# Performance work log

Measured on AMD Instinct MI355X. Metric: run time of the kernel, lower is better.

## Reference

```python
import jax, jax.numpy as jnp
import numpy as np

N = 100000      # nodes
E = 1_600_000   # edges (avg degree 16)
IN = 128
HID = 128
OUT = 64
C = 7           # num classes == K clusters
BETA = 1.0
NEG_SLOPE = 0.2


def setup_inputs() -> dict:
    key = jax.random.key(0)
    ks = jax.random.split(key, 12)
    x = jax.random.normal(ks[0], (N, IN), jnp.float32)
    edge_index = jax.random.randint(ks[1], (2, E), 0, N, dtype=jnp.int32)
    y = jax.random.randint(ks[2], (N,), 0, C, dtype=jnp.int32)
    C_b_prime = jax.random.normal(ks[3], (C, IN), jnp.float32)
    Q = jax.random.uniform(ks[4], (C, C), jnp.float32, 0.1, 1.0)  # positive, log-safe
    s1 = 1.0 / np.sqrt(IN)
    s2 = 1.0 / np.sqrt(HID)
    W1 = jax.random.uniform(ks[5], (IN, HID), jnp.float32, -s1, s1)
    a_src1 = jax.random.uniform(ks[6], (HID,), jnp.float32, -s2, s2)
    a_dst1 = jax.random.uniform(ks[7], (HID,), jnp.float32, -s2, s2)
    b1 = jnp.zeros((HID,), jnp.float32)
    W2 = jax.random.uniform(ks[8], (HID, OUT), jnp.float32, -s2, s2)
    b2 = jnp.zeros((OUT,), jnp.float32)
    return dict(x=x, edge_index=edge_index, y=y, C_b_prime=C_b_prime, Q=Q,
                W1=W1, a_src1=a_src1, a_dst1=a_dst1, b1=b1, W2=W2, b2=b2)


def _segment_softmax(logits, seg, num):
    m = jax.ops.segment_max(logits, seg, num_segments=num)
    e = jnp.exp(logits - m[seg])
    s = jax.ops.segment_sum(e, seg, num_segments=num)
    return e / (s[seg] + 1e-16)


def _clust_score(feat, cent, beta=BETA):
    # get_clust_score_pytorch: softmax-normalized exp(-beta * ||f - c_k||)
    d = jnp.linalg.norm(feat[:, None, :] - cent[None, :, :], axis=2)  # [N,K]
    sc = jnp.exp(-beta * d) + 1e-10
    return sc / sc.sum(1, keepdims=True)


def _gat_layer1(x, W, a_src, a_dst, b, src, dst):
    h = x @ W                                                   # F_0: [N,HID]
    logits = jax.nn.leaky_relu(h[src] @ a_src + h[dst] @ a_dst, NEG_SLOPE)  # [E]
    alpha = _segment_softmax(logits, dst, N)                    # B_0: [E]
    out = jax.ops.segment_sum(alpha[:, None] * h[src], dst, num_segments=N) + b  # Z_0
    return out, alpha, h


def reference(x, edge_index, y, C_b_prime, Q, W1, a_src1, a_dst1, b1, W2, b2):
    src, dst = edge_index[0], edge_index[1]

    # conv1 (GAT, heads=1) with return_attention_weights
    Z0, B0, F0 = _gat_layer1(x, W1, a_src1, a_dst1, b1, src, dst)
    x1 = jax.nn.elu(Z0)  # dropout p=0.5 in eval mode -> identity

    # ---- get_grad_IB_B_large ----
    y1h = jax.nn.one_hot(y, C, dtype=x.dtype)
    # run_kmeans(Z, y, C) replaced by detached class-mean centroids
    cnt = jax.ops.segment_sum(jnp.ones((N,), x.dtype), y, num_segments=C)
    C_a = jax.lax.stop_gradient(
        jax.ops.segment_sum(Z0, y, num_segments=C) / (cnt[:, None] + 1e-12))
    phi_Z = jax.lax.stop_gradient(_clust_score(Z0, C_a))      # [N,C], detached
    phi_X = _clust_score(x, C_b_prime)                        # [N,C]
    S = jnp.log(phi_X).sum(1)                                 # sum_b log phi_X_b
    diff_b = phi_Z * S[:, None] - y1h @ jnp.log(Q)            # [N,C]
    # U = d phi_Z / d Z (softmax-of-neg-distance Jacobian)
    dZ = Z0[:, None, :] - C_a[None, :, :]                     # [N,C,HID]
    dist = jnp.linalg.norm(dZ, axis=2, keepdims=True) + 1e-12
    g = -BETA * dZ / dist
    U = phi_Z[..., None] * (g - jnp.sum(phi_Z[..., None] * g, axis=1, keepdims=True))
    v = jnp.einsum('nkd,nk->nd', U, diff_b)                   # [N,HID]
    # grad_IB_B0[src,dst] = (v @ F0.T)[src,dst]/N, gathered per edge (no NxN dense)
    grad_e = jnp.einsum('ed,ed->e', v[src], F0[dst]) / N      # [E]

    B1 = B0 - grad_e
    # torch: B_1.norm(p=2, dim=1, keepdim=True) on [E,1] == |B_1| per edge, detached
    B1 = B1 / jax.lax.stop_gradient(jnp.abs(B1) + 1e-16)

    # conv2 with provided attention_weights B1
    h2 = x1 @ W2                                              # Z_1: [N,OUT]
    out = jax.ops.segment_sum(B1[:, None] * h2[src], dst, num_segments=N) + b2
    return out, h2, Z0, phi_Z
```

## Files before the change

kernel.cpp:

```cpp
#include <hip/hip_runtime.h>
#include <hip/hip_bf16.h>
#include <math.h>

#define IN_DIM 128
#define HID_DIM 128
#define OUT_DIM 64
#define NCLS 7

__global__ __launch_bounds__(256) void gemm1_kernel(
    const float* __restrict__ x, const float* __restrict__ W1,
    float* __restrict__ F0, int n) {
  __shared__ float xs[64 * 128];
  const int t = threadIdx.x;
  const int n0 = blockIdx.x * 64;

  for (int i = t; i < 64 * 128; i += 256) {
    int r = i >> 7, cc = i & 127;
    int gr = n0 + r;
    xs[i] = (gr < n) ? x[(size_t)gr * 128 + cc] : 0.0f;
  }
  __syncthreads();

  const int c = t & 127;
  const int half = t >> 7;
  float acc[32];
#pragma unroll
  for (int i = 0; i < 32; i++) acc[i] = 0.0f;

  for (int k0 = 0; k0 < 128; k0 += 8) {
    float w[8];
#pragma unroll
    for (int kk = 0; kk < 8; kk++) w[kk] = W1[(size_t)(k0 + kk) * 128 + c];
#pragma unroll
    for (int i = 0; i < 32; i++) {
      const int r = half + 2 * i;
#pragma unroll
      for (int kk = 0; kk < 8; kk++) acc[i] += xs[r * 128 + k0 + kk] * w[kk];
    }
  }
#pragma unroll
  for (int i = 0; i < 32; i++) {
    int gr = n0 + half + 2 * i;
    if (gr < n) F0[(size_t)gr * 128 + c] = acc[i];
  }
}

__global__ __launch_bounds__(256) void dots_kernel(
    const float* __restrict__ F0, const float* __restrict__ a_src,
    const float* __restrict__ a_dst, float* __restrict__ as_dot,
    float* __restrict__ ad_dot, int n) {
  const int wid = (blockIdx.x * blockDim.x + threadIdx.x) >> 6;
  const int lane = threadIdx.x & 63;
  if (wid >= n) return;
  float f0 = F0[(size_t)wid * 128 + lane];
  float f1 = F0[(size_t)wid * 128 + 64 + lane];
  float s = f0 * a_src[lane] + f1 * a_src[64 + lane];
  float d = f0 * a_dst[lane] + f1 * a_dst[64 + lane];
  for (int m = 32; m; m >>= 1) {
    s += __shfl_xor(s, m);
    d += __shfl_xor(d, m);
  }
  if (lane == 0) {
    as_dot[wid] = s;
    ad_dot[wid] = d;
  }
}

__global__ __launch_bounds__(256) void hist_kernel(const int* __restrict__ dst,
                                                   int* __restrict__ deg,
                                                   int e) {
  int i = blockIdx.x * blockDim.x + threadIdx.x;
  if (i < e) atomicAdd(&deg[dst[i]], 1);
}

__global__ __launch_bounds__(256) void scan1_kernel(const int* __restrict__ deg,
                                                    int* __restrict__ bsum,
                                                    int n) {
  __shared__ int lds[256];
  const int b = blockIdx.x, t = threadIdx.x;
  const int base = b * 1024 + t * 4;
  int s = 0;
#pragma unroll
  for (int u = 0; u < 4; u++) {
    int i = base + u;
    if (i < n) s += deg[i];
  }
  lds[t] = s;
  __syncthreads();
  for (int off = 128; off; off >>= 1) {
    if (t < off) lds[t] += lds[t + off];
    __syncthreads();
  }
  if (t == 0) bsum[b] = lds[0];
}

__global__ __launch_bounds__(1024) void scan2_kernel(
    const int* __restrict__ bsum, int* __restrict__ boff,
    int* __restrict__ rowptr, int nb, int n) {
  __shared__ int lds[1024];
  const int t = threadIdx.x;
  int v = (t < nb) ? bsum[t] : 0;
  lds[t] = v;
  __syncthreads();
  for (int off = 1; off < 1024; off <<= 1) {
    int add = (t >= off) ? lds[t - off] : 0;
    __syncthreads();
    lds[t] += add;
    __syncthreads();
  }
  if (t < nb) boff[t] = lds[t] - v;
  if (t == nb - 1) rowptr[n] = lds[t];
}

__global__ __launch_bounds__(256) void scan3_kernel(
    const int* __restrict__ deg, const int* __restrict__ boff,
    int* __restrict__ rowptr, int* __restrict__ cursor, int n) {
  __shared__ int lds[256];
  const int b = blockIdx.x, t = threadIdx.x;
  const int base = b * 1024 + t * 4;
  int v[4];
  int s = 0;
#pragma unroll
  for (int u = 0; u < 4; u++) {
    int i = base + u;
    v[u] = (i < n) ? deg[i] : 0;
    s += v[u];
  }
  lds[t] = s;
  __syncthreads();
  for (int off = 1; off < 256; off <<= 1) {
    int add = (t >= off) ? lds[t - off] : 0;
    __syncthreads();
    lds[t] += add;
    __syncthreads();
  }
  int run = boff[b] + lds[t] - s;
#pragma unroll
  for (int u = 0; u < 4; u++) {
    int i = base + u;
    if (i < n) {
      rowptr[i] = run;
      cursor[i] = run;
      run += v[u];
    }
  }
}

__global__ __launch_bounds__(256) void scatter_kernel(
    const int* __restrict__ src, const int* __restrict__ dst,
    int* __restrict__ cursor, int* __restrict__ esrc, int e) {
  int i = blockIdx.x * blockDim.x + threadIdx.x;
  if (i < e) {
    int pos = atomicAdd(&cursor[dst[i]], 1);
    esrc[pos] = src[i];
  }
}

__global__ __launch_bounds__(256) void gat1_kernel(
    const float* __restrict__ F0, const float* __restrict__ as_dot,
    const float* __restrict__ ad_dot, const int* __restrict__ rowptr,
    const int* __restrict__ esrc, const float* __restrict__ b1,
    float* __restrict__ alpha, float* __restrict__ Z0out, int n) {
  const int wid = (blockIdx.x * blockDim.x + threadIdx.x) >> 6;
  const int lane = threadIdx.x & 63;
  if (wid >= n) return;
  const int start = rowptr[wid];
  const int end = rowptr[wid + 1];
  const float adn = ad_dot[wid];

  float lmax = -INFINITY;
  for (int j = start + lane; j < end; j += 64) {
    int s = esrc[j];
    float z = as_dot[s] + adn;
    z = (z > 0.0f) ? z : 0.2f * z;
    lmax = fmaxf(lmax, z);
  }
  for (int m = 32; m; m >>= 1) lmax = fmaxf(lmax, __shfl_xor(lmax, m));

  float lsum = 0.0f;
  for (int j = start + lane; j < end; j += 64) {
    int s = esrc[j];
    float z = as_dot[s] + adn;
    z = (z > 0.0f) ? z : 0.2f * z;
    lsum += expf(z - lmax);
  }
  for (int m = 32; m; m >>= 1) lsum += __shfl_xor(lsum, m);
  const float inv = 1.0f / (lsum + 1e-16f);

  float acc0 = 0.0f, acc1 = 0.0f;
  for (int base = start; base < end; base += 64) {
    const int len = min(64, end - base);
    float aj = 0.0f;
    int sj = 0;
    if (lane < len) {
      int j = base + lane;
      sj = esrc[j];
      float z = as_dot[sj] + adn;
      z = (z > 0.0f) ? z : 0.2f * z;
      aj = expf(z - lmax) * inv;
      alpha[j] = aj;
    }
    for (int q = 0; q < len; q++) {
      float a = __shfl(aj, q);
      int s = __shfl(sj, q);
      acc0 += a * F0[(size_t)s * 128 + lane];
      acc1 += a * F0[(size_t)s * 128 + 64 + lane];
    }
  }
  Z0out[(size_t)wid * 128 + lane] = acc0 + b1[lane];
  Z0out[(size_t)wid * 128 + 64 + lane] = acc1 + b1[64 + lane];
}

#define CNB 256
__global__ __launch_bounds__(128) void centroid_partial_kernel(
    const float* __restrict__ Z0out, const int* __restrict__ y,
    float* __restrict__ partial, float* __restrict__ ccnt, int n, int per) {
  const int t = threadIdx.x;
  const int b = blockIdx.x;
  const int n0 = b * per;
  const int n1 = min(n0 + per, n);
  float a[NCLS];
#pragma unroll
  for (int k = 0; k < NCLS; k++) a[k] = 0.0f;
  int cnt[NCLS];
#pragma unroll
  for (int k = 0; k < NCLS; k++) cnt[k] = 0;

#pragma unroll 4
  for (int i = n0; i < n1; i++) {
    const int c = y[i];
    const float v = Z0out[(size_t)i * 128 + t];
#pragma unroll
    for (int k = 0; k < NCLS; k++) a[k] += (c == k) ? v : 0.0f;
    if (t == 0) {
#pragma unroll
      for (int k = 0; k < NCLS; k++) cnt[k] += (c == k) ? 1 : 0;
    }
  }
#pragma unroll
  for (int k = 0; k < NCLS; k++)
    partial[((size_t)b * NCLS + k) * 128 + t] = a[k];
  if (t == 0) {
#pragma unroll
    for (int k = 0; k < NCLS; k++) atomicAdd(&ccnt[k], (float)cnt[k]);
  }
}

__global__ __launch_bounds__(1024) void centroid_reduce_kernel(
    const float* __restrict__ partial, const float* __restrict__ ccnt,
    float* __restrict__ ca, int nb) {
  const int t = threadIdx.x;
  if (t >= NCLS * 128) return;
  float s = 0.0f;
#pragma unroll 8
  for (int b = 0; b < nb; b++) s += partial[(size_t)b * (NCLS * 128) + t];
  ca[t] = s / (ccnt[t >> 7] + 1e-12f);
}

__global__ __launch_bounds__(256) void phi_v_kernel(
    const float* __restrict__ Z0out, const float* __restrict__ x,
    const float* __restrict__ ca, const float* __restrict__ cb,
    const float* __restrict__ Q, const int* __restrict__ y,
    float* __restrict__ vbuf, float* __restrict__ phi_out, int n) {
  const int wid = (blockIdx.x * blockDim.x + threadIdx.x) >> 6;
  const int lane = threadIdx.x & 63;
  if (wid >= n) return;
  const float z0 = Z0out[(size_t)wid * 128 + lane];
  const float z1 = Z0out[(size_t)wid * 128 + 64 + lane];
  const float x0 = x[(size_t)wid * 128 + lane];
  const float x1 = x[(size_t)wid * 128 + 64 + lane];

  float sZ[NCLS], sX[NCLS];
#pragma unroll
  for (int k = 0; k < NCLS; k++) {
    float d0 = z0 - ca[k * 128 + lane];
    float d1 = z1 - ca[k * 128 + 64 + lane];
    sZ[k] = d0 * d0 + d1 * d1;
    float e0 = x0 - cb[k * 128 + lane];
    float e1 = x1 - cb[k * 128 + 64 + lane];
    sX[k] = e0 * e0 + e1 * e1;
  }
  for (int m = 32; m; m >>= 1) {
#pragma unroll
    for (int k = 0; k < NCLS; k++) {
      sZ[k] += __shfl_xor(sZ[k], m);
      sX[k] += __shfl_xor(sX[k], m);
    }
  }
  float distZ[NCLS], phiZ[NCLS];
  float sumZ = 0.0f, sumX = 0.0f, S = 0.0f;
#pragma unroll
  for (int k = 0; k < NCLS; k++) {
    distZ[k] = sqrtf(sZ[k]);
    float sc = expf(-distZ[k]) + 1e-10f;
    phiZ[k] = sc;
    sumZ += sc;
    float dx = sqrtf(sX[k]);
    float scx = expf(-dx) + 1e-10f;
    S += logf(scx);
    sumX += scx;
  }
  S -= 7.0f * logf(sumX);
  const float invZ = 1.0f / sumZ;
#pragma unroll
  for (int k = 0; k < NCLS; k++) phiZ[k] *= invZ;

  const int yc = y[wid];
  float w[NCLS];
  float W = 0.0f;
#pragma unroll
  for (int k = 0; k < NCLS; k++) {
    float diff = phiZ[k] * S - logf(Q[yc * NCLS + k]);
    w[k] = phiZ[k] * diff;
    W += w[k];
  }
  float v0 = 0.0f, v1 = 0.0f;
#pragma unroll
  for (int k = 0; k < NCLS; k++) {
    float coef = -(w[k] - W * phiZ[k]) / (distZ[k] + 1e-12f);
    v0 += coef * (z0 - ca[k * 128 + lane]);
    v1 += coef * (z1 - ca[k * 128 + 64 + lane]);
  }
  vbuf[(size_t)wid * 128 + lane] = v0;
  vbuf[(size_t)wid * 128 + 64 + lane] = v1;

  if (lane < NCLS) {
    float pv = (lane == 0) ? phiZ[0]
              : (lane == 1) ? phiZ[1]
              : (lane == 2) ? phiZ[2]
              : (lane == 3) ? phiZ[3]
              : (lane == 4) ? phiZ[4]
              : (lane == 5) ? phiZ[5]
                            : phiZ[6];
    phi_out[(size_t)wid * NCLS + lane] = pv;
  }
}

__global__ __launch_bounds__(256) void gemm2_kernel(
    const float* __restrict__ Z0out, const float* __restrict__ W2,
    float* __restrict__ h2, int n) {
  __shared__ float w2s[128 * 64];
  __shared__ float xs[16 * 128];
  const int t = threadIdx.x;
  for (int i = t; i < 128 * 64; i += 256) w2s[i] = W2[i];
  const int n0 = blockIdx.x * 16;
  for (int i = t; i < 16 * 128; i += 256) {
    int r = i >> 7, cc = i & 127;
    int gr = n0 + r;
    float zv = (gr < n) ? Z0out[(size_t)gr * 128 + cc] : 0.0f;
    xs[i] = (zv > 0.0f) ? zv : (expf(zv) - 1.0f);
  }
  __syncthreads();
  const int c = t & 63;
  const int rb = t >> 6;
  float acc[4] = {0.0f, 0.0f, 0.0f, 0.0f};
  for (int k = 0; k < 128; k++) {
    float wv = w2s[k * 64 + c];
#pragma unroll
    for (int i = 0; i < 4; i++) acc[i] += xs[(rb + 4 * i) * 128 + k] * wv;
  }
#pragma unroll
  for (int i = 0; i < 4; i++) {
    int gr = n0 + rb + 4 * i;
    if (gr < n) h2[(size_t)gr * 64 + c] = acc[i];
  }
}

__global__ __launch_bounds__(256) void conv2_kernel(
    const float* __restrict__ F0, const float* __restrict__ vbuf,
    const float* __restrict__ h2, const float* __restrict__ alpha,
    const int* __restrict__ rowptr, const int* __restrict__ esrc,
    const float* __restrict__ b2, float* __restrict__ outp, int n,
    float invN) {
  const int wid = (blockIdx.x * blockDim.x + threadIdx.x) >> 6;
  const int lane = threadIdx.x & 63;
  if (wid >= n) return;
  const int start = rowptr[wid];
  const int end = rowptr[wid + 1];
  const float f0 = F0[(size_t)wid * 128 + lane];
  const float f1 = F0[(size_t)wid * 128 + 64 + lane];
  float acc = 0.0f;
  for (int j = start; j < end; j++) {
    const int s = esrc[j];
    const float a = alpha[j];
    float p = vbuf[(size_t)s * 128 + lane] * f0 +
              vbuf[(size_t)s * 128 + 64 + lane] * f1;
    for (int m = 32; m; m >>= 1) p += __shfl_xor(p, m);
    const float B1 = a - p * invN;
    const float wgt = B1 / (fabsf(B1) + 1e-16f);
    acc += wgt * h2[(size_t)s * 64 + lane];
  }
  outp[(size_t)wid * 64 + lane] = acc + b2[lane];
}

extern "C" void kernel_launch(void* const* d_in, const int* in_sizes, int n_in,
                              void* d_out, int out_size, void* d_ws,
                              size_t ws_size, hipStream_t stream) {
  const float* x = (const float*)d_in[0];
  const int* ei = (const int*)d_in[1];
  const int* y = (const int*)d_in[2];
  const float* cb = (const float*)d_in[3];
  const float* Q = (const float*)d_in[4];
  const float* W1 = (const float*)d_in[5];
  const float* a_src = (const float*)d_in[6];
  const float* a_dst = (const float*)d_in[7];
  const float* b1 = (const float*)d_in[8];
  const float* W2 = (const float*)d_in[9];
  const float* b2 = (const float*)d_in[10];

  const int N = in_sizes[2];
  const int E = in_sizes[1] / 2;
  const int* srcp = ei;
  const int* dstp = ei + E;

  float* F0 = (float*)d_ws;
  float* as_dot = F0 + (size_t)N * 128;
  float* ad_dot = as_dot + N;
  float* alpha = ad_dot + N;
  float* vbuf = alpha + E;
  float* ca = vbuf + (size_t)N * 128;
  float* ccnt = ca + NCLS * 128;
  int* deg = (int*)(ccnt + 16);
  int* rowptr = deg + N;
  int* cursor = rowptr + N + 1;
  int* esrc = cursor + N;

  float* partial = vbuf;
  int* bsum = (int*)(vbuf + (size_t)CNB * NCLS * 128);
  int* boff = bsum + 1024;

  float* out_o = (float*)d_out;
  float* h2_o = out_o + (size_t)N * 64;
  float* z0_o = h2_o + (size_t)N * 64;
  float* phi_o = z0_o + (size_t)N * 128;

  hipMemsetAsync(deg, 0, (size_t)N * sizeof(int), stream);
  hipMemsetAsync(ccnt, 0, 16 * sizeof(float), stream);

  gemm1_kernel<<<(N + 63) / 64, 256, 0, stream>>>(x, W1, F0, N);
  dots_kernel<<<(N + 3) / 4, 256, 0, stream>>>(F0, a_src, a_dst, as_dot,
                                               ad_dot, N);
  hist_kernel<<<(E + 255) / 256, 256, 0, stream>>>(dstp, deg, E);
  {
    const int nb = (N + 1023) / 1024;
    scan1_kernel<<<nb, 256, 0, stream>>>(deg, bsum, N);
    scan2_kernel<<<1, 1024, 0, stream>>>(bsum, boff, rowptr, nb, N);
    scan3_kernel<<<nb, 256, 0, stream>>>(deg, boff, rowptr, cursor, N);
  }
  scatter_kernel<<<(E + 255) / 256, 256, 0, stream>>>(srcp, dstp, cursor, esrc,
                                                      E);
  gat1_kernel<<<(N + 3) / 4, 256, 0, stream>>>(F0, as_dot, ad_dot, rowptr,
                                               esrc, b1, alpha, z0_o, N);
  {
    const int per = (N + CNB - 1) / CNB;
    centroid_partial_kernel<<<CNB, 128, 0, stream>>>(z0_o, y, partial, ccnt, N,
                                                     per);
    centroid_reduce_kernel<<<1, 1024, 0, stream>>>(partial, ccnt, ca, CNB);
  }
  phi_v_kernel<<<(N + 3) / 4, 256, 0, stream>>>(z0_o, x, ca, cb, Q, y, vbuf,
                                                phi_o, N);
  gemm2_kernel<<<(N + 15) / 16, 256, 0, stream>>>(z0_o, W2, h2_o, N);
  conv2_kernel<<<(N + 3) / 4, 256, 0, stream>>>(F0, vbuf, h2_o, alpha, rowptr,
                                                esrc, b2, out_o, N,
                                                1.0f / (float)N);
}
```

Measured before the change: 1.105 ms.

## Process four edges per wavefront with float4 gathers in GAT aggregation and conv2

The conv1 aggregation and conv2 kernels now split each 64-lane wavefront into four 16-lane groups. Each group handles one edge and loads its 128-float row with float4 vector loads, and the groups' partial sums are combined by cross-group shuffles. In conv2 the per-edge dot product becomes a 4-step intra-group reduction instead of a 6-step full-wave one, and the h2 gather reuses the broadcast weights. The aim is more memory-level parallelism and fewer shuffles and serial iterations per edge. The cost is extra reduction shuffles at the end and wasted lanes when a node's degree is not a multiple of four.

New measurement: 1.030 ms. 1.07x faster.

```diff
diff --git a/kernel.cpp b/kernel.cpp
--- a/kernel.cpp
+++ b/kernel.cpp
@@ -187,28 +187,43 @@
   for (int m = 32; m; m >>= 1) lsum += __shfl_xor(lsum, m);
   const float inv = 1.0f / (lsum + 1e-16f);
 
-  float acc0 = 0.0f, acc1 = 0.0f;
-  for (int base = start; base < end; base += 64) {
-    const int len = min(64, end - base);
+  const int g = lane >> 4;
+  const int l = lane & 15;
+  float4 accA = {0.f, 0.f, 0.f, 0.f};
+  float4 accB = {0.f, 0.f, 0.f, 0.f};
+  for (int base = start; base < end; base += 4) {
+    const int j = base + g;
+    const bool act = (j < end);
+    const int sj = act ? esrc[j] : 0;
     float aj = 0.0f;
-    int sj = 0;
-    if (lane < len) {
-      int j = base + lane;
-      sj = esrc[j];
+    if (act) {
       float z = as_dot[sj] + adn;
       z = (z > 0.0f) ? z : 0.2f * z;
       aj = expf(z - lmax) * inv;
-      alpha[j] = aj;
-    }
-    for (int q = 0; q < len; q++) {
-      float a = __shfl(aj, q);
-      int s = __shfl(sj, q);
-      acc0 += a * F0[(size_t)s * 128 + lane];
-      acc1 += a * F0[(size_t)s * 128 + 64 + lane];
-    }
-  }
-  Z0out[(size_t)wid * 128 + lane] = acc0 + b1[lane];
-  Z0out[(size_t)wid * 128 + 64 + lane] = acc1 + b1[64 + lane];
+      if (l == 0) alpha[j] = aj;
+    }
+    const float4 vA = *(const float4*)&F0[(size_t)sj * 128 + l * 8];
+    const float4 vB = *(const float4*)&F0[(size_t)sj * 128 + l * 8 + 4];
+    accA.x += aj * vA.x; accA.y += aj * vA.y;
+    accA.z += aj * vA.z; accA.w += aj * vA.w;
+    accB.x += aj * vB.x; accB.y += aj * vB.y;
+    accB.z += aj * vB.z; accB.w += aj * vB.w;
+  }
+#pragma unroll
+  for (int m = 16; m <= 32; m <<= 1) {
+    accA.x += __shfl_xor(accA.x, m); accA.y += __shfl_xor(accA.y, m);
+    accA.z += __shfl_xor(accA.z, m); accA.w += __shfl_xor(accA.w, m);
+    accB.x += __shfl_xor(accB.x, m); accB.y += __shfl_xor(accB.y, m);
+    accB.z += __shfl_xor(accB.z, m); accB.w += __shfl_xor(accB.w, m);
+  }
+  if (g == 0) {
+    const float4 bA = *(const float4*)&b1[l * 8];
+    const float4 bB = *(const float4*)&b1[l * 8 + 4];
+    float4 oA = {accA.x + bA.x, accA.y + bA.y, accA.z + bA.z, accA.w + bA.w};
+    float4 oB = {accB.x + bB.x, accB.y + bB.y, accB.z + bB.z, accB.w + bB.w};
+    *(float4*)&Z0out[(size_t)wid * 128 + l * 8] = oA;
+    *(float4*)&Z0out[(size_t)wid * 128 + l * 8 + 4] = oB;
+  }
 }
 
 #define CNB 256
@@ -377,18 +392,32 @@
   if (wid >= n) return;
   const int start = rowptr[wid];
   const int end = rowptr[wid + 1];
-  const float f0 = F0[(size_t)wid * 128 + lane];
-  const float f1 = F0[(size_t)wid * 128 + 64 + lane];
+  const int g = lane >> 4;
+  const int l = lane & 15;
+  const float4 fA = *(const float4*)&F0[(size_t)wid * 128 + l * 8];
+  const float4 fB = *(const float4*)&F0[(size_t)wid * 128 + l * 8 + 4];
   float acc = 0.0f;
-  for (int j = start; j < end; j++) {
-    const int s = esrc[j];
-    const float a = alpha[j];
-    float p = vbuf[(size_t)s * 128 + lane] * f0 +
-              vbuf[(size_t)s * 128 + 64 + lane] * f1;
-    for (int m = 32; m; m >>= 1) p += __shfl_xor(p, m);
+  for (int base = start; base < end; base += 4) {
+    const int j = base + g;
+    const bool act = (j < end);
+    const int sj = act ? esrc[j] : 0;
+    const float a = act ? alpha[j] : 0.0f;
+    const float4 vA = *(const float4*)&vbuf[(size_t)sj * 128 + l * 8];
+    const float4 vB = *(const float4*)&vbuf[(size_t)sj * 128 + l * 8 + 4];
+    float p = vA.x * fA.x + vA.y * fA.y + vA.z * fA.z + vA.w * fA.w +
+              vB.x * fB.x + vB.y * fB.y + vB.z * fB.z + vB.w * fB.w;
+    p += __shfl_xor(p, 1);
+    p += __shfl_xor(p, 2);
+    p += __shfl_xor(p, 4);
+    p += __shfl_xor(p, 8);
     const float B1 = a - p * invN;
-    const float wgt = B1 / (fabsf(B1) + 1e-16f);
-    acc += wgt * h2[(size_t)s * 64 + lane];
+    const float w = act ? (B1 / (fabsf(B1) + 1e-16f)) : 0.0f;
+#pragma unroll
+    for (int g2 = 0; g2 < 4; g2++) {
+      const float wg = __shfl(w, g2 * 16);
+      const int sg = __shfl(sj, g2 * 16);
+      acc += wg * h2[(size_t)sg * 64 + lane];
+    }
   }
   outp[(size_t)wid * 64 + lane] = acc + b2[lane];
 }
```
